# Kernel tuning notes

Measured on AMD Instinct MI355X. Metric: run time of the kernel, lower is better.

## Reference

```python
import jax, jax.numpy as jnp
import numpy as np

NUM_HEADS = 8
LN_EPS = 1e-5


def layer_norm_chw(x, w, b):
    # LayerNorm over (C, H, W) jointly, elementwise affine of shape (C, H, W)
    mu = jnp.mean(x, axis=(1, 2, 3), keepdims=True)
    var = jnp.mean(jnp.square(x - mu), axis=(1, 2, 3), keepdims=True)
    return (x - mu) * jax.lax.rsqrt(var + LN_EPS) * w[None] + b[None]


def conv1x1(x, w, b):
    # 1x1 conv == per-pixel matmul. x: (B,C,H,W), w: (O,C), b: (O,)
    return jnp.einsum('bcxy,oc->boxy', x, w) + b[None, :, None, None]


def setup_inputs() -> dict:
    key = jax.random.key(0)
    ks = jax.random.split(key, 8)
    B, C, H, W = 16, 512, 64, 64
    Dq, Dv, Dh = 512, 512, 2048
    s = lambda fan_in: 1.0 / np.sqrt(fan_in)
    return {
        'x': jax.random.normal(ks[0], (B, C, H, W), jnp.float32),
        'ln1_w': jnp.ones((C, H, W), jnp.float32),
        'ln1_b': jnp.zeros((C, H, W), jnp.float32),
        'q_w': jax.random.normal(ks[1], (Dq, C), jnp.float32) * s(C),
        'q_b': jnp.zeros((Dq,), jnp.float32),
        'k_w': jax.random.normal(ks[2], (Dq, C), jnp.float32) * s(C),
        'k_b': jnp.zeros((Dq,), jnp.float32),
        'v_w': jax.random.normal(ks[3], (Dv, C), jnp.float32) * s(C),
        'v_b': jnp.zeros((Dv,), jnp.float32),
        'hu_w': jax.random.normal(ks[4], (C, Dv), jnp.float32) * s(Dv),
        'hu_b': jnp.zeros((C,), jnp.float32),
        'ln2_w': jnp.ones((C, H, W), jnp.float32),
        'ln2_b': jnp.zeros((C, H, W), jnp.float32),
        'ff1_w': jax.random.normal(ks[5], (Dh, C), jnp.float32) * s(C),
        'ff1_b': jnp.zeros((Dh,), jnp.float32),
        'ff2_w': jax.random.normal(ks[6], (C, Dh), jnp.float32) * s(Dh),
        'ff2_b': jnp.zeros((C,), jnp.float32),
    }


def reference(x, ln1_w, ln1_b, q_w, q_b, k_w, k_b, v_w, v_b,
              hu_w, hu_b, ln2_w, ln2_b, ff1_w, ff1_b, ff2_w, ff2_b):
    B, C, H, W = x.shape
    h = NUM_HEADS

    a = layer_norm_chw(x, ln1_w, ln1_b)
    Q = conv1x1(a, q_w, q_b)   # (B, Dq, H, W)
    K = conv1x1(a, k_w, k_b)   # (B, Dq, H, W)
    V = conv1x1(a, v_w, v_b)   # (B, Dv, H, W)

    Dq, Dv = Q.shape[1], V.shape[1]
    # softmax over channel dim for Q (per pixel, over all Dq channels)
    Q = jax.nn.softmax(Q, axis=1)
    # softmax over flattened spatial dim for K (per channel)
    K = jax.nn.softmax(K.reshape(B, Dq, H * W), axis=-1).reshape(B, Dq, H, W)

    # split heads: (B, h, d, H, W)
    Qh = Q.reshape(B, h, Dq // h, H, W)
    Kh = K.reshape(B, h, Dq // h, H, W)
    Vh = V.reshape(B, h, Dv // h, H, W)

    # linear attention: KV = sum_xy K ⊗ V, then per-pixel KV^T @ Q
    KV = jnp.einsum('bhkxy,bhvxy->bhkv', Kh, Vh)        # (B, h, dq, dv)
    attn = jnp.einsum('bhkv,bhkxy->bhvxy', KV, Qh)      # (B, h, dv, H, W)
    attn = attn.reshape(B, Dv, H, W)
    attn = conv1x1(attn, hu_w, hu_b)                    # (B, C, H, W)

    x = x + attn
    x = layer_norm_chw(x, ln2_w, ln2_b)
    ff = conv1x1(jax.nn.gelu(conv1x1(x, ff1_w, ff1_b), approximate=False), ff2_w, ff2_b)
    return x + ff
```

## Files before the change

### kernel.cpp

```cpp
#include <hip/hip_runtime.h>
#include <math.h>

#define BATCH 16
#define CCH   512
#define HWS   4096
#define CHW   (CCH*HWS)
#define DHFF  2048
#define NHEAD 8
#define HD    64
#define QKVLD 1536
#define LNEPS 1e-5f

typedef unsigned short u16;
typedef __bf16 bf16x8 __attribute__((ext_vector_type(8)));
typedef float f32x4 __attribute__((ext_vector_type(4)));

__device__ __forceinline__ float gelu_f(float x) {
    float y = 1.5957691216057308f * x * (1.0f + 0.044715f * x * x);
    return x / (1.0f + __expf(-y));
}
__device__ __forceinline__ u16 f2bf(float f) {
    union { float f; unsigned u; } c; c.f = f;
    unsigned r = c.u + 0x7FFFu + ((c.u >> 16) & 1u);
    return (u16)(r >> 16);
}
__device__ __forceinline__ float bf2f(u16 h) {
    union { unsigned u; float f; } c; c.u = ((unsigned)h) << 16; return c.f;
}
__device__ __forceinline__ void gld16(const u16* g, u16* l) {
    __builtin_amdgcn_global_load_lds((const __attribute__((address_space(1))) unsigned*)g,
                                     (__attribute__((address_space(3))) unsigned*)l, 16, 0, 0);
}

__global__ __launch_bounds__(256) void stats_k(const float* __restrict__ src,
                                               float* __restrict__ st) {
    int b = blockIdx.y;
    const float4* p = (const float4*)(src + (size_t)b * CHW + (size_t)blockIdx.x * (CHW / 64));
    float s = 0.f, ss = 0.f;
    for (int i = threadIdx.x; i < (CHW / 64 / 4); i += 256) {
        float4 v = p[i];
        s  += v.x + v.y + v.z + v.w;
        ss += v.x * v.x + v.y * v.y + v.z * v.z + v.w * v.w;
    }
    __shared__ float r1[256], r2[256];
    int t = threadIdx.x;
    r1[t] = s; r2[t] = ss; __syncthreads();
    for (int o = 128; o > 0; o >>= 1) {
        if (t < o) { r1[t] += r1[t + o]; r2[t] += r2[t + o]; }
        __syncthreads();
    }
    if (t == 0) { atomicAdd(&st[2 * b], r1[0]); atomicAdd(&st[2 * b + 1], r2[0]); }
}

__global__ __launch_bounds__(256) void cvt_k(const float* __restrict__ src,
                                             u16* __restrict__ dst, int n4) {
    int i = blockIdx.x * 256 + threadIdx.x;
    if (i >= n4) return;
    float4 v = ((const float4*)src)[i];
    uint2 o; u16* op = (u16*)&o;
    op[0] = f2bf(v.x); op[1] = f2bf(v.y); op[2] = f2bf(v.z); op[3] = f2bf(v.w);
    ((uint2*)dst)[i] = o;
}

__global__ __launch_bounds__(256) void tr_k(const float* __restrict__ src,
                                            float* __restrict__ dst) {
    int p0 = blockIdx.x * 32, c0 = blockIdx.y * 32;
    __shared__ float T[32][33];
    int tx = threadIdx.x & 31, ty = threadIdx.x >> 5;
#pragma unroll
    for (int i = 0; i < 4; ++i)
        T[ty + i * 8][tx] = src[(size_t)(c0 + ty + i * 8) * HWS + p0 + tx];
    __syncthreads();
#pragma unroll
    for (int i = 0; i < 4; ++i)
        dst[(size_t)(p0 + ty + i * 8) * CCH + c0 + tx] = T[tx][ty + i * 8];
}

__global__ __launch_bounds__(256) void ln1t_k(const float* __restrict__ x,
                                              const float* __restrict__ w,
                                              const float* __restrict__ bb,
                                              const float* __restrict__ st,
                                              u16* __restrict__ a, int cb) {
    int p0 = blockIdx.x * 32, c0 = blockIdx.y * 32, bl = blockIdx.z;
    int b = cb + bl;
    float mean = st[2 * b] * (1.0f / CHW);
    float var  = st[2 * b + 1] * (1.0f / CHW) - mean * mean;
    float rstd = rsqrtf(var + LNEPS);
    __shared__ float T[32][33];
    int tx = threadIdx.x & 31, ty = threadIdx.x >> 5;
    const float* xb = x + (size_t)b * CHW;
#pragma unroll
    for (int i = 0; i < 4; ++i) {
        size_t o = (size_t)(c0 + ty + i * 8) * HWS + p0 + tx;
        T[ty + i * 8][tx] = (xb[o] - mean) * rstd * w[o] + bb[o];
    }
    __syncthreads();
    u16* ab = a + (size_t)bl * CHW;
#pragma unroll
    for (int i = 0; i < 4; ++i)
        ab[(size_t)(p0 + ty + i * 8) * CCH + c0 + tx] = f2bf(T[tx][ty + i * 8]);
}

template<int K, int ACT, int OBF>
__global__ __launch_bounds__(256) void gemm_tn(const u16* __restrict__ A,
                                               const u16* __restrict__ B,
                                               const float* __restrict__ bias,
                                               void* __restrict__ Out,
                                               int ldo, int nt) {
    __shared__ u16 As[2][128 * 32];
    __shared__ u16 Bs[2][128 * 32];
    const int tid = threadIdx.x;
    const int cpx = gridDim.x >> 3;
    const int wg = (blockIdx.x & 7) * cpx + (blockIdx.x >> 3);
    const int m0 = (wg / nt) * 128;
    const int n0 = (wg % nt) * 128;
    const int lane = tid & 63;
    const int w = tid >> 6;
    const int wm = (w & 1) * 64, wn = (w >> 1) * 64;
    const int ls = lane & 15, lq = lane >> 4;

    f32x4 acc[4][4];
#pragma unroll
    for (int i = 0; i < 4; ++i)
#pragma unroll
        for (int j = 0; j < 4; ++j) acc[i][j] = (f32x4){0.f, 0.f, 0.f, 0.f};

    const int srow = w * 16 + (lane >> 2);
    const int scol = (lane & 3) * 8;
    const u16* gA0 = A + (size_t)(m0 + srow) * K + scol;
    const u16* gA1 = gA0 + (size_t)64 * K;
    const u16* gB0 = B + (size_t)(n0 + srow) * K + scol;
    const u16* gB1 = gB0 + (size_t)64 * K;
    const int lo = w * 512;

    gld16(gA0, &As[0][lo]);
    gld16(gA1, &As[0][2048 + lo]);
    gld16(gB0, &Bs[0][lo]);
    gld16(gB1, &Bs[0][2048 + lo]);
    __syncthreads();

#pragma unroll 8
    for (int kt = 0; kt < K; kt += 32) {
        const int cur = (kt >> 5) & 1;
        const int nx = cur ^ 1;
        if (kt + 32 < K) {
            gld16(gA0 + kt + 32, &As[nx][lo]);
            gld16(gA1 + kt + 32, &As[nx][2048 + lo]);
            gld16(gB0 + kt + 32, &Bs[nx][lo]);
            gld16(gB1 + kt + 32, &Bs[nx][2048 + lo]);
        }
        bf16x8 af[4], bfv[4];
#pragma unroll
        for (int i = 0; i < 4; ++i)
            af[i] = *(bf16x8*)&As[cur][(wm + i * 16 + ls) * 32 + lq * 8];
#pragma unroll
        for (int j = 0; j < 4; ++j)
            bfv[j] = *(bf16x8*)&Bs[cur][(wn + j * 16 + ls) * 32 + lq * 8];
#pragma unroll
        for (int i = 0; i < 4; ++i)
#pragma unroll
            for (int j = 0; j < 4; ++j)
                acc[i][j] = __builtin_amdgcn_mfma_f32_16x16x32_bf16(bfv[j], af[i], acc[i][j], 0, 0, 0);
        if (kt + 32 < K)
            __syncthreads();
    }

#pragma unroll
    for (int j = 0; j < 4; ++j) {
        int nb = n0 + wn + j * 16 + lq * 4;
        float4 bv = *(const float4*)&bias[nb];
#pragma unroll
        for (int i = 0; i < 4; ++i) {
            int m = m0 + wm + i * 16 + ls;
            float v0 = acc[i][j][0] + bv.x;
            float v1 = acc[i][j][1] + bv.y;
            float v2 = acc[i][j][2] + bv.z;
            float v3 = acc[i][j][3] + bv.w;
            if (ACT) { v0 = gelu_f(v0); v1 = gelu_f(v1); v2 = gelu_f(v2); v3 = gelu_f(v3); }
            size_t idx = (size_t)m * ldo + nb;
            if (OBF) {
                uint2 o; u16* op = (u16*)&o;
                op[0] = f2bf(v0); op[1] = f2bf(v1); op[2] = f2bf(v2); op[3] = f2bf(v3);
                *(uint2*)((u16*)Out + idx) = o;
            } else {
                *(float4*)((float*)Out + idx) = (float4){v0, v1, v2, v3};
            }
        }
    }
}

__global__ __launch_bounds__(256) void softmax_row_k(u16* __restrict__ QKV) {
    int m = blockIdx.x * 4 + (threadIdx.x >> 6);
    int lane = threadIdx.x & 63;
    u16* row = QKV + (size_t)m * QKVLD + lane * 8;
    uint4 raw = *(uint4*)row;
    u16* pr = (u16*)&raw;
    float v[8];
#pragma unroll
    for (int i = 0; i < 8; ++i) v[i] = bf2f(pr[i]);
    float mx = v[0];
#pragma unroll
    for (int i = 1; i < 8; ++i) mx = fmaxf(mx, v[i]);
    for (int o = 32; o > 0; o >>= 1) mx = fmaxf(mx, __shfl_xor(mx, o, 64));
    float s = 0.f;
#pragma unroll
    for (int i = 0; i < 8; ++i) { v[i] = __expf(v[i] - mx); s += v[i]; }
    for (int o = 32; o > 0; o >>= 1) s += __shfl_xor(s, o, 64);
    float inv = 1.0f / s;
#pragma unroll
    for (int i = 0; i < 8; ++i) pr[i] = f2bf(v[i] * inv);
    *(uint4*)row = raw;
}

__global__ __launch_bounds__(256) void kcolstat_k(const u16* __restrict__ QKV,
                                                  float* __restrict__ kpart) {
    int pc = blockIdx.x, bl = blockIdx.y;
    int cg = threadIdx.x & 63;
    int ps = threadIdx.x >> 6;
    const u16* base = QKV + (size_t)bl * HWS * QKVLD + CCH + cg * 8;
    int p0 = pc * 256 + ps * 64;
    float m[8];
#pragma unroll
    for (int i = 0; i < 8; ++i) m[i] = -1e30f;
    for (int p = p0; p < p0 + 64; ++p) {
        uint4 r = *(const uint4*)(base + (size_t)p * QKVLD);
        u16* rp = (u16*)&r;
#pragma unroll
        for (int i = 0; i < 8; ++i) m[i] = fmaxf(m[i], bf2f(rp[i]));
    }
    __shared__ float red[4][512];
#pragma unroll
    for (int i = 0; i < 8; ++i) red[ps][cg * 8 + i] = m[i];
    __syncthreads();
#pragma unroll
    for (int i = 0; i < 8; ++i)
        m[i] = fmaxf(fmaxf(red[0][cg * 8 + i], red[1][cg * 8 + i]),
                     fmaxf(red[2][cg * 8 + i], red[3][cg * 8 + i]));
    __syncthreads();
    float s[8];
#pragma unroll
    for (int i = 0; i < 8; ++i) s[i] = 0.f;
    for (int p = p0; p < p0 + 64; ++p) {
        uint4 r = *(const uint4*)(base + (size_t)p * QKVLD);
        u16* rp = (u16*)&r;
#pragma unroll
        for (int i = 0; i < 8; ++i) s[i] += __expf(bf2f(rp[i]) - m[i]);
    }
#pragma unroll
    for (int i = 0; i < 8; ++i) red[ps][cg * 8 + i] = s[i];
    __syncthreads();
    if (ps == 0) {
        float* outp = kpart + (((size_t)bl * 16 + pc) * 512 + cg * 8) * 2;
#pragma unroll
        for (int i = 0; i < 8; ++i) {
            float sv = red[0][cg * 8 + i] + red[1][cg * 8 + i] +
                       red[2][cg * 8 + i] + red[3][cg * 8 + i];
            outp[2 * i] = m[i]; outp[2 * i + 1] = sv;
        }
    }
}

__global__ __launch_bounds__(256) void kcolmerge_k(const float* __restrict__ kpart,
                                                   float* __restrict__ kstat) {
    int bl = blockIdx.x;
#pragma unroll
    for (int j = 0; j < 2; ++j) {
        int col = threadIdx.x * 2 + j;
        float m = -1e30f;
        for (int pc = 0; pc < 16; ++pc)
            m = fmaxf(m, kpart[(((size_t)bl * 16 + pc) * 512 + col) * 2]);
        float s = 0.f;
        for (int pc = 0; pc < 16; ++pc) {
            const float* p = kpart + (((size_t)bl * 16 + pc) * 512 + col) * 2;
            s += p[1] * __expf(p[0] - m);
        }
        kstat[((size_t)bl * 512 + col) * 2]     = m;
        kstat[((size_t)bl * 512 + col) * 2 + 1] = 1.0f / s;
    }
}

__global__ __launch_bounds__(256) void kv_k2(const u16* __restrict__ QKV,
                                             const float* __restrict__ kstat,
                                             float* __restrict__ KV) {
    int pc = blockIdx.x, h = blockIdx.y, bl = blockIdx.z;
    const u16* kbase = QKV + (size_t)bl * HWS * QKVLD + CCH + h * HD;
    const u16* vbase = kbase + CCH;
    float* kvb = KV + ((size_t)bl * NHEAD + h) * (HD * HD);
    __shared__ float Ks[64][65], Vs[64][65];
    __shared__ float Ms[64], Is[64];
    int tid = threadIdx.x;
    if (tid < 64) {
        const float* sp = kstat + ((size_t)bl * 512 + h * HD + tid) * 2;
        Ms[tid] = sp[0]; Is[tid] = sp[1];
    }
    int tk = tid >> 4, tv = tid & 15;
    float acc[4][4];
#pragma unroll
    for (int i = 0; i < 4; ++i)
#pragma unroll
        for (int j = 0; j < 4; ++j) acc[i][j] = 0.f;

    for (int s = 0; s < 4; ++s) {
        int pbase = pc * 256 + s * 64;
        __syncthreads();
#pragma unroll
        for (int j = 0; j < 2; ++j) {
            int li = tid + j * 256;
            int pl = li >> 3, c8 = (li & 7) * 8;
            uint4 kr = *(const uint4*)(kbase + (size_t)(pbase + pl) * QKVLD + c8);
            uint4 vr = *(const uint4*)(vbase + (size_t)(pbase + pl) * QKVLD + c8);
            u16* kp = (u16*)&kr; u16* vp = (u16*)&vr;
#pragma unroll
            for (int t = 0; t < 8; ++t) {
                Ks[pl][c8 + t] = __expf(bf2f(kp[t]) - Ms[c8 + t]) * Is[c8 + t];
                Vs[pl][c8 + t] = bf2f(vp[t]);
            }
        }
        __syncthreads();
#pragma unroll 4
        for (int p = 0; p < 64; ++p) {
            float ka[4], va[4];
#pragma unroll
            for (int i = 0; i < 4; ++i) { ka[i] = Ks[p][tk * 4 + i]; va[i] = Vs[p][tv * 4 + i]; }
#pragma unroll
            for (int i = 0; i < 4; ++i)
#pragma unroll
                for (int j = 0; j < 4; ++j) acc[i][j] += ka[i] * va[j];
        }
    }
#pragma unroll
    for (int i = 0; i < 4; ++i)
#pragma unroll
        for (int j = 0; j < 4; ++j)
            atomicAdd(&kvb[(size_t)(tk * 4 + i) * HD + tv * 4 + j], acc[i][j]);
}

__global__ __launch_bounds__(256) void attn_k2(const u16* __restrict__ QKV,
                                               const float* __restrict__ KV,
                                               u16* __restrict__ attnRaw) {
    int pt = blockIdx.x, h = blockIdx.y, bl = blockIdx.z;
    const u16* qbase = QKV + (size_t)bl * HWS * QKVLD + h * HD;
    const float* kvb = KV + ((size_t)bl * NHEAD + h) * (HD * HD);
    __shared__ float KVs[64][68], Qs[64][68];
    int tid = threadIdx.x;
#pragma unroll
    for (int j = 0; j < 4; ++j) {
        int li = tid + j * 256;
        int k = li >> 4, c4 = (li & 15) * 4;
        *(float4*)&KVs[k][c4] = *(const float4*)(kvb + (size_t)k * HD + c4);
    }
#pragma unroll
    for (int j = 0; j < 2; ++j) {
        int li = tid + j * 256;
        int pl = li >> 3, c8 = (li & 7) * 8;
        uint4 qr = *(const uint4*)(qbase + (size_t)(pt * 64 + pl) * QKVLD + c8);
        u16* qp = (u16*)&qr;
#pragma unroll
        for (int t = 0; t < 8; ++t) Qs[pl][c8 + t] = bf2f(qp[t]);
    }
    __syncthreads();
    int tp = tid >> 4, tv = tid & 15;
    float acc[4][4];
#pragma unroll
    for (int i = 0; i < 4; ++i)
#pragma unroll
        for (int j = 0; j < 4; ++j) acc[i][j] = 0.f;
#pragma unroll 4
    for (int k = 0; k < 64; ++k) {
        float qa[4], kv4[4];
#pragma unroll
        for (int i = 0; i < 4; ++i) { qa[i] = Qs[tp * 4 + i][k]; kv4[i] = KVs[k][tv * 4 + i]; }
#pragma unroll
        for (int i = 0; i < 4; ++i)
#pragma unroll
            for (int j = 0; j < 4; ++j) acc[i][j] += qa[i] * kv4[j];
    }
#pragma unroll
    for (int i = 0; i < 4; ++i) {
        uint2 wv; u16* wp = (u16*)&wv;
#pragma unroll
        for (int j = 0; j < 4; ++j) wp[j] = f2bf(acc[i][j]);
        *(uint2*)(attnRaw + (size_t)(bl * HWS + pt * 64 + tp * 4 + i) * CCH + h * HD + tv * 4) = wv;
    }
}

__global__ __launch_bounds__(256) void resid_t_k(const float* __restrict__ x,
                                                 const float* __restrict__ ao,
                                                 float* __restrict__ r,
                                                 float* __restrict__ pstat, int cb) {
    int p0 = blockIdx.x * 32, c0 = blockIdx.y * 32, bl = blockIdx.z;
    int b = cb + bl;
    __shared__ float T[32][33];
    __shared__ float r1[256], r2[256];
    int tx = threadIdx.x & 31, ty = threadIdx.x >> 5;
    const float* xb = x + (size_t)b * CHW;
#pragma unroll
    for (int i = 0; i < 4; ++i)
        T[ty + i * 8][tx] = xb[(size_t)(c0 + ty + i * 8) * HWS + p0 + tx];
    __syncthreads();
    float s = 0.f, ss = 0.f;
#pragma unroll
    for (int i = 0; i < 4; ++i) {
        size_t o = (size_t)bl * CHW + (size_t)(p0 + ty + i * 8) * CCH + c0 + tx;
        float v = T[tx][ty + i * 8] + ao[o];
        r[o] = v; s += v; ss += v * v;
    }
    int t = threadIdx.x;
    r1[t] = s; r2[t] = ss; __syncthreads();
    for (int o = 128; o > 0; o >>= 1) {
        if (t < o) { r1[t] += r1[t + o]; r2[t] += r2[t + o]; }
        __syncthreads();
    }
    if (t == 0) {
        float* pp = pstat + ((size_t)b * 2048 + (size_t)blockIdx.x * 16 + blockIdx.y) * 2;
        pp[0] = r1[0]; pp[1] = r2[0];
    }
}

__global__ __launch_bounds__(256) void red2_k(const float* __restrict__ pstat,
                                              float* __restrict__ st, int cb) {
    int b = cb + blockIdx.x;
    const float* p = pstat + (size_t)b * 4096;
    float s = 0.f, ss = 0.f;
    for (int i = threadIdx.x; i < 2048; i += 256) {
        s += p[2 * i]; ss += p[2 * i + 1];
    }
    __shared__ float r1[256], r2[256];
    int t = threadIdx.x;
    r1[t] = s; r2[t] = ss; __syncthreads();
    for (int o = 128; o > 0; o >>= 1) {
        if (t < o) { r1[t] += r1[t + o]; r2[t] += r2[t + o]; }
        __syncthreads();
    }
    if (t == 0) { st[32 + 2 * b] = r1[0]; st[32 + 2 * b + 1] = r2[0]; }
}

__global__ __launch_bounds__(256) void ln2a_k(const float* __restrict__ r,
                                              const float* __restrict__ w2t,
                                              const float* __restrict__ b2t,
                                              const float* __restrict__ st,
                                              u16* __restrict__ x2, int cb) {
    size_t i4 = (size_t)blockIdx.x * 256 + threadIdx.x;
    int bl = (int)(i4 / (CHW / 4));
    int b = cb + bl;
    size_t off4 = i4 % (CHW / 4);
    float mean = st[32 + 2 * b] * (1.0f / CHW);
    float var  = st[32 + 2 * b + 1] * (1.0f / CHW) - mean * mean;
    float rstd = rsqrtf(var + LNEPS);
    float4 v  = ((const float4*)(r + (size_t)bl * CHW))[off4];
    float4 wv = ((const float4*)w2t)[off4];
    float4 bv = ((const float4*)b2t)[off4];
    uint2 o; u16* op = (u16*)&o;
    op[0] = f2bf((v.x - mean) * rstd * wv.x + bv.x);
    op[1] = f2bf((v.y - mean) * rstd * wv.y + bv.y);
    op[2] = f2bf((v.z - mean) * rstd * wv.z + bv.z);
    op[3] = f2bf((v.w - mean) * rstd * wv.w + bv.w);
    ((uint2*)(x2 + (size_t)bl * CHW))[off4] = o;
}

__global__ __launch_bounds__(256) void final_t_k(const u16* __restrict__ x2,
                                                 const float* __restrict__ ffo,
                                                 float* __restrict__ out, int cb) {
    int c0 = blockIdx.x * 32, p0 = blockIdx.y * 32, bl = blockIdx.z;
    int b = cb + bl;
    __shared__ float T[32][33];
    int tx = threadIdx.x & 31, ty = threadIdx.x >> 5;
#pragma unroll
    for (int i = 0; i < 4; ++i) {
        size_t o = (size_t)bl * CHW + (size_t)(p0 + ty + i * 8) * CCH + c0 + tx;
        T[ty + i * 8][tx] = ffo[o] + bf2f(x2[o]);
    }
    __syncthreads();
    float* ob = out + (size_t)b * CHW;
#pragma unroll
    for (int i = 0; i < 4; ++i)
        ob[(size_t)(c0 + ty + i * 8) * HWS + p0 + tx] = T[tx][ty + i * 8];
}

extern "C" void kernel_launch(void* const* d_in, const int* in_sizes, int n_in,
                              void* d_out, int out_size, void* d_ws, size_t ws_size,
                              hipStream_t stream) {
    const float* x    = (const float*)d_in[0];
    const float* ln1w = (const float*)d_in[1];
    const float* ln1b = (const float*)d_in[2];
    const float* qw   = (const float*)d_in[3];
    const float* qb   = (const float*)d_in[4];
    const float* kw   = (const float*)d_in[5];
    const float* kb   = (const float*)d_in[6];
    const float* vw   = (const float*)d_in[7];
    const float* vb   = (const float*)d_in[8];
    const float* huw  = (const float*)d_in[9];
    const float* hub  = (const float*)d_in[10];
    const float* ln2w = (const float*)d_in[11];
    const float* ln2b = (const float*)d_in[12];
    const float* f1w  = (const float*)d_in[13];
    const float* f1b  = (const float*)d_in[14];
    const float* f2w  = (const float*)d_in[15];
    const float* f2b  = (const float*)d_in[16];
    float* out = (float*)d_out;
    float* ws = (float*)d_ws;

    float* stats = ws;
    float* qkvb  = ws + 64;
    u16*   wqkv  = (u16*)(ws + 1600);
    u16*   whu   = (u16*)(ws + 394816);
    u16*   wf1   = (u16*)(ws + 525888);
    u16*   wf2   = (u16*)(ws + 1050176);
    float* w2t   = ws + 1574464;
    float* b2t   = ws + 3671616;
    float* pstat = ws + 5768768;
    float* kpart = ws + 5834304;
    float* kstat = ws + 6096448;
    float* kvbuf = ws + 6112832;

    int G = 16;
    while (G > 1 && (6112832ull + (size_t)G * 7372800ull) * 4ull > ws_size) G >>= 1;
    const int nch = BATCH / G;
    const size_t U = (size_t)G * CHW;

    float* R       = kvbuf + (size_t)G * 32768;
    u16*   a_bf    = (u16*)R;
    u16*   QKVb    = (u16*)(R + U / 2);
    float* attnOut = R + U / 2;
    float* rbuf    = R + 3 * U / 2;
    u16*   x2bf    = (u16*)R;
    u16*   Hbuf    = (u16*)(R + U / 2);
    float* ffOut   = R + 5 * U / 2;

    hipMemsetAsync(stats, 0, 64 * sizeof(float), stream);

    cvt_k<<<dim3(256), 256, 0, stream>>>(qw, wqkv, 65536);
    cvt_k<<<dim3(256), 256, 0, stream>>>(kw, wqkv + 262144, 65536);
    cvt_k<<<dim3(256), 256, 0, stream>>>(vw, wqkv + 524288, 65536);
    cvt_k<<<dim3(256), 256, 0, stream>>>(huw, whu, 65536);
    cvt_k<<<dim3(1024), 256, 0, stream>>>(f1w, wf1, 262144);
    cvt_k<<<dim3(1024), 256, 0, stream>>>(f2w, wf2, 262144);
    tr_k<<<dim3(128, 16), 256, 0, stream>>>(ln2w, w2t);
    tr_k<<<dim3(128, 16), 256, 0, stream>>>(ln2b, b2t);
    hipMemcpyAsync(qkvb,        qb, 512 * sizeof(float), hipMemcpyDeviceToDevice, stream);
    hipMemcpyAsync(qkvb + 512,  kb, 512 * sizeof(float), hipMemcpyDeviceToDevice, stream);
    hipMemcpyAsync(qkvb + 1024, vb, 512 * sizeof(float), hipMemcpyDeviceToDevice, stream);

    stats_k<<<dim3(64, BATCH), 256, 0, stream>>>(x, stats);

    for (int g = 0; g < nch; ++g) {
        const int cb = g * G;
        const int mt = G * 32;
        ln1t_k<<<dim3(128, 16, G), 256, 0, stream>>>(x, ln1w, ln1b, stats, a_bf, cb);
        gemm_tn<512, 0, 1><<<dim3(mt * 12), 256, 0, stream>>>(a_bf, wqkv, qkvb, QKVb, QKVLD, 12);
        softmax_row_k<<<dim3(G * 1024), 256, 0, stream>>>(QKVb);
        kcolstat_k<<<dim3(16, G), 256, 0, stream>>>(QKVb, kpart);
        kcolmerge_k<<<dim3(G), 256, 0, stream>>>(kpart, kstat);
        hipMemsetAsync(kvbuf, 0, (size_t)G * 32768 * sizeof(float), stream);
        kv_k2<<<dim3(16, NHEAD, G), 256, 0, stream>>>(QKVb, kstat, kvbuf);
        attn_k2<<<dim3(64, NHEAD, G), 256, 0, stream>>>(QKVb, kvbuf, a_bf);
        gemm_tn<512, 0, 0><<<dim3(mt * 4), 256, 0, stream>>>(a_bf, whu, hub, attnOut, CCH, 4);
        resid_t_k<<<dim3(128, 16, G), 256, 0, stream>>>(x, attnOut, rbuf, pstat, cb);
        red2_k<<<dim3(G), 256, 0, stream>>>(pstat, stats, cb);
        ln2a_k<<<dim3(G * 2048), 256, 0, stream>>>(rbuf, w2t, b2t, stats, x2bf, cb);
        gemm_tn<512, 1, 1><<<dim3(mt * 16), 256, 0, stream>>>(x2bf, wf1, f1b, Hbuf, DHFF, 16);
        gemm_tn<2048, 0, 0><<<dim3(mt * 4), 256, 0, stream>>>(Hbuf, wf2, f2b, ffOut, CCH, 4);
        final_t_k<<<dim3(16, 128, G), 256, 0, stream>>>(x2bf, ffOut, out, cb);
    }
}
```

Baseline: 1.500 ms.

## Fuse residual and LN stats into hu GEMM, residual+transpose into FF2 GEMM

The hidden-update GEMM epilogue now adds the input residual (read transposed from x), writes the pixel-major residual buffer and per-tile LayerNorm partial sums, so the separate residual kernel disappears. The FF2 GEMM epilogue adds the bf16 LN2 output, transposes through shared memory and writes the final channel-major output, so the fp32 ffOut round trip and the final transpose kernel are gone. The red2 reduction shrinks to 128 partials, and the workspace requirement drops, which may allow larger batch chunks. The trade-off is that the hu epilogue reads x with strided, uncoalesced loads, and the FF2 epilogue adds extra shared-memory passes.

After: 1.451 ms. 3.3% less time.

```diff
diff --git a/kernel.cpp b/kernel.cpp
--- a/kernel.cpp
+++ b/kernel.cpp
@@ -27,9 +27,72 @@
 __device__ __forceinline__ float bf2f(u16 h) {
     union { unsigned u; float f; } c; c.u = ((unsigned)h) << 16; return c.f;
 }
+__device__ __forceinline__ uint2 pack_bf16x4(float v0, float v1, float v2, float v3) {
+    union { uint2 u; __bf16 b[4]; } o;
+    o.b[0] = (__bf16)v0; o.b[1] = (__bf16)v1; o.b[2] = (__bf16)v2; o.b[3] = (__bf16)v3;
+    return o.u;
+}
 __device__ __forceinline__ void gld16(const u16* g, u16* l) {
     __builtin_amdgcn_global_load_lds((const __attribute__((address_space(1))) unsigned*)g,
                                      (__attribute__((address_space(3))) unsigned*)l, 16, 0, 0);
+}
+
+template<int K>
+__device__ __forceinline__ void gemm_core(const u16* __restrict__ A,
+                                          const u16* __restrict__ B,
+                                          int m0, int n0,
+                                          u16 (&As)[2][128 * 32],
+                                          u16 (&Bs)[2][128 * 32],
+                                          f32x4 (&acc)[4][4]) {
+    const int tid = threadIdx.x;
+    const int lane = tid & 63;
+    const int w = tid >> 6;
+    const int wm = (w & 1) * 64, wn = (w >> 1) * 64;
+    const int ls = lane & 15, lq = lane >> 4;
+#pragma unroll
+    for (int i = 0; i < 4; ++i)
+#pragma unroll
+        for (int j = 0; j < 4; ++j) acc[i][j] = (f32x4){0.f, 0.f, 0.f, 0.f};
+
+    const int srow = w * 16 + (lane >> 2);
+    const int scol = (lane & 3) * 8;
+    const u16* gA0 = A + (size_t)(m0 + srow) * K + scol;
+    const u16* gA1 = gA0 + (size_t)64 * K;
+    const u16* gB0 = B + (size_t)(n0 + srow) * K + scol;
+    const u16* gB1 = gB0 + (size_t)64 * K;
+    const int lo = w * 512;
+
+    gld16(gA0, &As[0][lo]);
+    gld16(gA1, &As[0][2048 + lo]);
+    gld16(gB0, &Bs[0][lo]);
+    gld16(gB1, &Bs[0][2048 + lo]);
+    __syncthreads();
+
+#pragma unroll 8
+    for (int kt = 0; kt < K; kt += 32) {
+        const int cur = (kt >> 5) & 1;
+        const int nx = cur ^ 1;
+        if (kt + 32 < K) {
+            gld16(gA0 + kt + 32, &As[nx][lo]);
+            gld16(gA1 + kt + 32, &As[nx][2048 + lo]);
+            gld16(gB0 + kt + 32, &Bs[nx][lo]);
+            gld16(gB1 + kt + 32, &Bs[nx][2048 + lo]);
+        }
+        bf16x8 af[4], bfv[4];
+#pragma unroll
+        for (int i = 0; i < 4; ++i)
+            af[i] = *(bf16x8*)&As[cur][(wm + i * 16 + ls) * 32 + lq * 8];
+#pragma unroll
+        for (int j = 0; j < 4; ++j)
+            bfv[j] = *(bf16x8*)&Bs[cur][(wn + j * 16 + ls) * 32 + lq * 8];
+#pragma unroll
+        for (int i = 0; i < 4; ++i)
+#pragma unroll
+            for (int j = 0; j < 4; ++j)
+                acc[i][j] = __builtin_amdgcn_mfma_f32_16x16x32_bf16(bfv[j], af[i], acc[i][j], 0, 0, 0);
+        if (kt + 32 < K)
+            __syncthreads();
+    }
 }
 
 __global__ __launch_bounds__(256) void stats_k(const float* __restrict__ src,
@@ -57,9 +120,7 @@
     int i = blockIdx.x * 256 + threadIdx.x;
     if (i >= n4) return;
     float4 v = ((const float4*)src)[i];
-    uint2 o; u16* op = (u16*)&o;
-    op[0] = f2bf(v.x); op[1] = f2bf(v.y); op[2] = f2bf(v.z); op[3] = f2bf(v.w);
-    ((uint2*)dst)[i] = o;
+    ((uint2*)dst)[i] = pack_bf16x4(v.x, v.y, v.z, v.w);
 }
 
 __global__ __launch_bounds__(256) void tr_k(const float* __restrict__ src,
@@ -101,70 +162,25 @@
         ab[(size_t)(p0 + ty + i * 8) * CCH + c0 + tx] = f2bf(T[tx][ty + i * 8]);
 }
 
-template<int K, int ACT, int OBF>
+template<int K, int ACT>
 __global__ __launch_bounds__(256) void gemm_tn(const u16* __restrict__ A,
                                                const u16* __restrict__ B,
                                                const float* __restrict__ bias,
-                                               void* __restrict__ Out,
+                                               u16* __restrict__ Out,
                                                int ldo, int nt) {
     __shared__ u16 As[2][128 * 32];
     __shared__ u16 Bs[2][128 * 32];
-    const int tid = threadIdx.x;
     const int cpx = gridDim.x >> 3;
-    const int wg = (blockIdx.x & 7) * cpx + (blockIdx.x >> 3);
+    const int wg = ((int)blockIdx.x & 7) * cpx + ((int)blockIdx.x >> 3);
     const int m0 = (wg / nt) * 128;
     const int n0 = (wg % nt) * 128;
-    const int lane = tid & 63;
-    const int w = tid >> 6;
+    f32x4 acc[4][4];
+    gemm_core<K>(A, B, m0, n0, As, Bs, acc);
+
+    const int lane = threadIdx.x & 63;
+    const int w = threadIdx.x >> 6;
     const int wm = (w & 1) * 64, wn = (w >> 1) * 64;
     const int ls = lane & 15, lq = lane >> 4;
-
-    f32x4 acc[4][4];
-#pragma unroll
-    for (int i = 0; i < 4; ++i)
-#pragma unroll
-        for (int j = 0; j < 4; ++j) acc[i][j] = (f32x4){0.f, 0.f, 0.f, 0.f};
-
-    const int srow = w * 16 + (lane >> 2);
-    const int scol = (lane & 3) * 8;
-    const u16* gA0 = A + (size_t)(m0 + srow) * K + scol;
-    const u16* gA1 = gA0 + (size_t)64 * K;
-    const u16* gB0 = B + (size_t)(n0 + srow) * K + scol;
-    const u16* gB1 = gB0 + (size_t)64 * K;
-    const int lo = w * 512;
-
-    gld16(gA0, &As[0][lo]);
-    gld16(gA1, &As[0][2048 + lo]);
-    gld16(gB0, &Bs[0][lo]);
-    gld16(gB1, &Bs[0][2048 + lo]);
-    __syncthreads();
-
-#pragma unroll 8
-    for (int kt = 0; kt < K; kt += 32) {
-        const int cur = (kt >> 5) & 1;
-        const int nx = cur ^ 1;
-        if (kt + 32 < K) {
-            gld16(gA0 + kt + 32, &As[nx][lo]);
-            gld16(gA1 + kt + 32, &As[nx][2048 + lo]);
-            gld16(gB0 + kt + 32, &Bs[nx][lo]);
-            gld16(gB1 + kt + 32, &Bs[nx][2048 + lo]);
-        }
-        bf16x8 af[4], bfv[4];
-#pragma unroll
-        for (int i = 0; i < 4; ++i)
-            af[i] = *(bf16x8*)&As[cur][(wm + i * 16 + ls) * 32 + lq * 8];
-#pragma unroll
-        for (int j = 0; j < 4; ++j)
-            bfv[j] = *(bf16x8*)&Bs[cur][(wn + j * 16 + ls) * 32 + lq * 8];
-#pragma unroll
-        for (int i = 0; i < 4; ++i)
-#pragma unroll
-            for (int j = 0; j < 4; ++j)
-                acc[i][j] = __builtin_amdgcn_mfma_f32_16x16x32_bf16(bfv[j], af[i], acc[i][j], 0, 0, 0);
-        if (kt + 32 < K)
-            __syncthreads();
-    }
-
 #pragma unroll
     for (int j = 0; j < 4; ++j) {
         int nb = n0 + wn + j * 16 + lq * 4;
@@ -177,15 +193,122 @@
             float v2 = acc[i][j][2] + bv.z;
             float v3 = acc[i][j][3] + bv.w;
             if (ACT) { v0 = gelu_f(v0); v1 = gelu_f(v1); v2 = gelu_f(v2); v3 = gelu_f(v3); }
-            size_t idx = (size_t)m * ldo + nb;
-            if (OBF) {
-                uint2 o; u16* op = (u16*)&o;
-                op[0] = f2bf(v0); op[1] = f2bf(v1); op[2] = f2bf(v2); op[3] = f2bf(v3);
-                *(uint2*)((u16*)Out + idx) = o;
-            } else {
-                *(float4*)((float*)Out + idx) = (float4){v0, v1, v2, v3};
+            *(uint2*)(Out + (size_t)m * ldo + nb) = pack_bf16x4(v0, v1, v2, v3);
+        }
+    }
+}
+
+__global__ __launch_bounds__(256) void gemm_hu_resid(const u16* __restrict__ A,
+                                                     const u16* __restrict__ B,
+                                                     const float* __restrict__ bias,
+                                                     float* __restrict__ r,
+                                                     const float* __restrict__ x,
+                                                     float* __restrict__ pstat, int cb) {
+    __shared__ u16 As[2][128 * 32];
+    __shared__ u16 Bs[2][128 * 32];
+    __shared__ float r1[256], r2[256];
+    const int nt = 4;
+    const int cpx = gridDim.x >> 3;
+    const int wg = ((int)blockIdx.x & 7) * cpx + ((int)blockIdx.x >> 3);
+    const int m0 = (wg / nt) * 128;
+    const int n0 = (wg % nt) * 128;
+    f32x4 acc[4][4];
+    gemm_core<512>(A, B, m0, n0, As, Bs, acc);
+
+    const int lane = threadIdx.x & 63;
+    const int w = threadIdx.x >> 6;
+    const int wm = (w & 1) * 64, wn = (w >> 1) * 64;
+    const int ls = lane & 15, lq = lane >> 4;
+    const int bl = m0 >> 12;
+    const int p0loc = m0 & 4095;
+    const float* xb = x + (size_t)(cb + bl) * CHW;
+    float* rb = r + (size_t)bl * CHW;
+    float s = 0.f, ss = 0.f;
+#pragma unroll
+    for (int j = 0; j < 4; ++j) {
+        int nb = n0 + wn + j * 16 + lq * 4;
+        float4 bv = *(const float4*)&bias[nb];
+#pragma unroll
+        for (int i = 0; i < 4; ++i) {
+            int p = p0loc + wm + i * 16 + ls;
+            float v0 = acc[i][j][0] + bv.x + xb[(size_t)(nb + 0) * HWS + p];
+            float v1 = acc[i][j][1] + bv.y + xb[(size_t)(nb + 1) * HWS + p];
+            float v2 = acc[i][j][2] + bv.z + xb[(size_t)(nb + 2) * HWS + p];
+            float v3 = acc[i][j][3] + bv.w + xb[(size_t)(nb + 3) * HWS + p];
+            *(float4*)(rb + (size_t)p * CCH + nb) = (float4){v0, v1, v2, v3};
+            s  += v0 + v1 + v2 + v3;
+            ss += v0 * v0 + v1 * v1 + v2 * v2 + v3 * v3;
+        }
+    }
+    int t = threadIdx.x;
+    __syncthreads();
+    r1[t] = s; r2[t] = ss; __syncthreads();
+    for (int o = 128; o > 0; o >>= 1) {
+        if (t < o) { r1[t] += r1[t + o]; r2[t] += r2[t + o]; }
+        __syncthreads();
+    }
+    if (t == 0) {
+        int slot = ((p0loc >> 7) << 2) + (wg % nt);
+        float* pp = pstat + ((size_t)(cb + bl) * 128 + slot) * 2;
+        pp[0] = r1[0]; pp[1] = r2[0];
+    }
+}
+
+__global__ __launch_bounds__(256) void gemm_ff2_final(const u16* __restrict__ A,
+                                                      const u16* __restrict__ B,
+                                                      const float* __restrict__ bias,
+                                                      float* __restrict__ out,
+                                                      const u16* __restrict__ x2,
+                                                      int cb) {
+    __shared__ union {
+        struct { u16 As[2][128 * 32]; u16 Bs[2][128 * 32]; } g;
+        float Tt[64][130];
+    } shm;
+    const int nt = 4;
+    const int cpx = gridDim.x >> 3;
+    const int wg = ((int)blockIdx.x & 7) * cpx + ((int)blockIdx.x >> 3);
+    const int m0 = (wg / nt) * 128;
+    const int n0 = (wg % nt) * 128;
+    f32x4 acc[4][4];
+    gemm_core<2048>(A, B, m0, n0, shm.g.As, shm.g.Bs, acc);
+
+    const int tid = threadIdx.x;
+    const int lane = tid & 63;
+    const int w = tid >> 6;
+    const int wm = (w & 1) * 64, wn = (w >> 1) * 64;
+    const int ls = lane & 15, lq = lane >> 4;
+    const int bl = m0 >> 12;
+    const int p0loc = m0 & 4095;
+    const u16* x2b = x2 + (size_t)bl * CHW;
+    float* ob = out + (size_t)(cb + bl) * CHW;
+
+    const int row = tid >> 2, mc = (tid & 3) * 32;
+#pragma unroll
+    for (int rnd = 0; rnd < 2; ++rnd) {
+        __syncthreads();
+        if ((wn >> 6) == rnd) {
+#pragma unroll
+            for (int j = 0; j < 4; ++j) {
+                int nloc = wn + j * 16 + lq * 4;
+                float4 bv = *(const float4*)&bias[n0 + nloc];
+#pragma unroll
+                for (int i = 0; i < 4; ++i) {
+                    int m = wm + i * 16 + ls;
+                    uint2 xr = *(const uint2*)&x2b[(size_t)(p0loc + m) * CCH + n0 + nloc];
+                    u16* xp = (u16*)&xr;
+                    int tr = nloc & 63;
+                    shm.Tt[tr + 0][m] = acc[i][j][0] + bv.x + bf2f(xp[0]);
+                    shm.Tt[tr + 1][m] = acc[i][j][1] + bv.y + bf2f(xp[1]);
+                    shm.Tt[tr + 2][m] = acc[i][j][2] + bv.z + bf2f(xp[2]);
+                    shm.Tt[tr + 3][m] = acc[i][j][3] + bv.w + bf2f(xp[3]);
+                }
             }
         }
+        __syncthreads();
+        float* orow = ob + (size_t)(n0 + rnd * 64 + row) * HWS + p0loc + mc;
+#pragma unroll
+        for (int q = 0; q < 32; q += 4)
+            *(float4*)(orow + q) = *(float4*)&shm.Tt[row][mc + q];
     }
 }
 
@@ -377,62 +500,22 @@
     }
 #pragma unroll
     for (int i = 0; i < 4; ++i) {
-        uint2 wv; u16* wp = (u16*)&wv;
-#pragma unroll
-        for (int j = 0; j < 4; ++j) wp[j] = f2bf(acc[i][j]);
-        *(uint2*)(attnRaw + (size_t)(bl * HWS + pt * 64 + tp * 4 + i) * CCH + h * HD + tv * 4) = wv;
-    }
-}
-
-__global__ __launch_bounds__(256) void resid_t_k(const float* __restrict__ x,
-                                                 const float* __restrict__ ao,
-                                                 float* __restrict__ r,
-                                                 float* __restrict__ pstat, int cb) {
-    int p0 = blockIdx.x * 32, c0 = blockIdx.y * 32, bl = blockIdx.z;
-    int b = cb + bl;
-    __shared__ float T[32][33];
-    __shared__ float r1[256], r2[256];
-    int tx = threadIdx.x & 31, ty = threadIdx.x >> 5;
-    const float* xb = x + (size_t)b * CHW;
-#pragma unroll
-    for (int i = 0; i < 4; ++i)
-        T[ty + i * 8][tx] = xb[(size_t)(c0 + ty + i * 8) * HWS + p0 + tx];
-    __syncthreads();
-    float s = 0.f, ss = 0.f;
-#pragma unroll
-    for (int i = 0; i < 4; ++i) {
-        size_t o = (size_t)bl * CHW + (size_t)(p0 + ty + i * 8) * CCH + c0 + tx;
-        float v = T[tx][ty + i * 8] + ao[o];
-        r[o] = v; s += v; ss += v * v;
-    }
-    int t = threadIdx.x;
-    r1[t] = s; r2[t] = ss; __syncthreads();
-    for (int o = 128; o > 0; o >>= 1) {
-        if (t < o) { r1[t] += r1[t + o]; r2[t] += r2[t + o]; }
-        __syncthreads();
-    }
-    if (t == 0) {
-        float* pp = pstat + ((size_t)b * 2048 + (size_t)blockIdx.x * 16 + blockIdx.y) * 2;
-        pp[0] = r1[0]; pp[1] = r2[0];
-    }
-}
-
-__global__ __launch_bounds__(256) void red2_k(const float* __restrict__ pstat,
+        *(uint2*)(attnRaw + (size_t)(bl * HWS + pt * 64 + tp * 4 + i) * CCH + h * HD + tv * 4) =
+            pack_bf16x4(acc[i][0], acc[i][1], acc[i][2], acc[i][3]);
+    }
+}
+
+__global__ __launch_bounds__(128) void red2_k(const float* __restrict__ pstat,
                                               float* __restrict__ st, int cb) {
     int b = cb + blockIdx.x;
-    const float* p = pstat + (size_t)b * 4096;
-    float s = 0.f, ss = 0.f;
-    for (int i = threadIdx.x; i < 2048; i += 256) {
-        s += p[2 * i]; ss += p[2 * i + 1];
-    }
-    __shared__ float r1[256], r2[256];
+    const float* p = pstat + (size_t)b * 256;
     int t = threadIdx.x;
-    r1[t] = s; r2[t] = ss; __syncthreads();
-    for (int o = 128; o > 0; o >>= 1) {
-        if (t < o) { r1[t] += r1[t + o]; r2[t] += r2[t + o]; }
-        __syncthreads();
-    }
-    if (t == 0) { st[32 + 2 * b] = r1[0]; st[32 + 2 * b + 1] = r2[0]; }
+    float s = p[2 * t], ss = p[2 * t + 1];
+    for (int o = 32; o > 0; o >>= 1) { s += __shfl_down(s, o, 64); ss += __shfl_down(ss, o, 64); }
+    __shared__ float sh[4];
+    if ((t & 63) == 0) { sh[(t >> 6) * 2] = s; sh[(t >> 6) * 2 + 1] = ss; }
+    __syncthreads();
+    if (t == 0) { st[32 + 2 * b] = sh[0] + sh[2]; st[32 + 2 * b + 1] = sh[1] + sh[3]; }
 }
 
 __global__ __launch_bounds__(256) void ln2a_k(const float* __restrict__ r,
@@ -450,31 +533,11 @@
     float4 v  = ((const float4*)(r + (size_t)bl * CHW))[off4];
     float4 wv = ((const float4*)w2t)[off4];
     float4 bv = ((const float4*)b2t)[off4];
-    uint2 o; u16* op = (u16*)&o;
-    op[0] = f2bf((v.x - mean) * rstd * wv.x + bv.x);
-    op[1] = f2bf((v.y - mean) * rstd * wv.y + bv.y);
-    op[2] = f2bf((v.z - mean) * rstd * wv.z + bv.z);
-    op[3] = f2bf((v.w - mean) * rstd * wv.w + bv.w);
-    ((uint2*)(x2 + (size_t)bl * CHW))[off4] = o;
-}
-
-__global__ __launch_bounds__(256) void final_t_k(const u16* __restrict__ x2,
-                                                 const float* __restrict__ ffo,
-                                                 float* __restrict__ out, int cb) {
-    int c0 = blockIdx.x * 32, p0 = blockIdx.y * 32, bl = blockIdx.z;
-    int b = cb + bl;
-    __shared__ float T[32][33];
-    int tx = threadIdx.x & 31, ty = threadIdx.x >> 5;
-#pragma unroll
-    for (int i = 0; i < 4; ++i) {
-        size_t o = (size_t)bl * CHW + (size_t)(p0 + ty + i * 8) * CCH + c0 + tx;
-        T[ty + i * 8][tx] = ffo[o] + bf2f(x2[o]);
-    }
-    __syncthreads();
-    float* ob = out + (size_t)b * CHW;
-#pragma unroll
-    for (int i = 0; i < 4; ++i)
-        ob[(size_t)(c0 + ty + i * 8) * HWS + p0 + tx] = T[tx][ty + i * 8];
+    ((uint2*)(x2 + (size_t)bl * CHW))[off4] =
+        pack_bf16x4((v.x - mean) * rstd * wv.x + bv.x,
+                    (v.y - mean) * rstd * wv.y + bv.y,
+                    (v.z - mean) * rstd * wv.z + bv.z,
+                    (v.w - mean) * rstd * wv.w + bv.w);
 }
 
 extern "C" void kernel_launch(void* const* d_in, const int* in_sizes, int n_in,
@@ -514,18 +577,16 @@
     float* kvbuf = ws + 6112832;
 
     int G = 16;
-    while (G > 1 && (6112832ull + (size_t)G * 7372800ull) * 4ull > ws_size) G >>= 1;
+    while (G > 1 && (6112832ull + (size_t)G * 5275648ull) * 4ull > ws_size) G >>= 1;
     const int nch = BATCH / G;
     const size_t U = (size_t)G * CHW;
 
     float* R       = kvbuf + (size_t)G * 32768;
     u16*   a_bf    = (u16*)R;
     u16*   QKVb    = (u16*)(R + U / 2);
-    float* attnOut = R + U / 2;
     float* rbuf    = R + 3 * U / 2;
     u16*   x2bf    = (u16*)R;
     u16*   Hbuf    = (u16*)(R + U / 2);
-    float* ffOut   = R + 5 * U / 2;
 
     hipMemsetAsync(stats, 0, 64 * sizeof(float), stream);
 
@@ -547,19 +608,17 @@
         const int cb = g * G;
         const int mt = G * 32;
         ln1t_k<<<dim3(128, 16, G), 256, 0, stream>>>(x, ln1w, ln1b, stats, a_bf, cb);
-        gemm_tn<512, 0, 1><<<dim3(mt * 12), 256, 0, stream>>>(a_bf, wqkv, qkvb, QKVb, QKVLD, 12);
+        gemm_tn<512, 0><<<dim3(mt * 12), 256, 0, stream>>>(a_bf, wqkv, qkvb, QKVb, QKVLD, 12);
         softmax_row_k<<<dim3(G * 1024), 256, 0, stream>>>(QKVb);
         kcolstat_k<<<dim3(16, G), 256, 0, stream>>>(QKVb, kpart);
         kcolmerge_k<<<dim3(G), 256, 0, stream>>>(kpart, kstat);
         hipMemsetAsync(kvbuf, 0, (size_t)G * 32768 * sizeof(float), stream);
         kv_k2<<<dim3(16, NHEAD, G), 256, 0, stream>>>(QKVb, kstat, kvbuf);
         attn_k2<<<dim3(64, NHEAD, G), 256, 0, stream>>>(QKVb, kvbuf, a_bf);
-        gemm_tn<512, 0, 0><<<dim3(mt * 4), 256, 0, stream>>>(a_bf, whu, hub, attnOut, CCH, 4);
-        resid_t_k<<<dim3(128, 16, G), 256, 0, stream>>>(x, attnOut, rbuf, pstat, cb);
-        red2_k<<<dim3(G), 256, 0, stream>>>(pstat, stats, cb);
+        gemm_hu_resid<<<dim3(mt * 4), 256, 0, stream>>>(a_bf, whu, hub, rbuf, x, pstat, cb);
+        red2_k<<<dim3(G), 128, 0, stream>>>(pstat, stats, cb);
         ln2a_k<<<dim3(G * 2048), 256, 0, stream>>>(rbuf, w2t, b2t, stats, x2bf, cb);
-        gemm_tn<512, 1, 1><<<dim3(mt * 16), 256, 0, stream>>>(x2bf, wf1, f1b, Hbuf, DHFF, 16);
-        gemm_tn<2048, 0, 0><<<dim3(mt * 4), 256, 0, stream>>>(Hbuf, wf2, f2b, ffOut, CCH, 4);
-        final_t_k<<<dim3(16, 128, G), 256, 0, stream>>>(x2bf, ffOut, out, cb);
-    }
-}
+        gemm_tn<512, 1><<<dim3(mt * 16), 256, 0, stream>>>(x2bf, wf1, f1b, Hbuf, DHFF, 16);
+        gemm_ff2_final<<<dim3(mt * 4), 256, 0, stream>>>(Hbuf, wf2, f2b, out, x2bf, cb);
+    }
+}
```
